# Kernel tuning notes

Hardware: AMD Instinct MI355X
Metric: run time of the kernel (lower is better)

## Reference

```python
import jax, jax.numpy as jnp
import numpy as np

H, L, N = 128, 8192, 64


def setup_inputs() -> dict:
    key = jax.random.key(0)
    ks = jax.random.split(key, 8)
    u = jax.random.normal(ks[0], (H, L), jnp.float32)
    # lecun_normal-scaled params, per channel
    Ct_ri = jax.random.normal(ks[1], (H, N, 2), jnp.float32) / np.sqrt(N)
    B_raw = jax.random.normal(ks[2], (H, N, 1), jnp.float32) / np.sqrt(N)
    D = jax.random.uniform(ks[3], (H,), jnp.float32)
    lo, hi = np.log(0.001), np.log(0.1)
    log_step = jax.random.uniform(ks[4], (H,), jnp.float32) * (hi - lo) + lo
    n = np.arange(N, dtype=np.float32)
    Lambda_re = jnp.full((N,), -0.5, jnp.float32)
    Lambda_im = jnp.asarray(np.pi * n, jnp.float32)
    p_re = jnp.asarray(np.sqrt(n + 0.5), jnp.float32)
    p_im = jnp.zeros((N,), jnp.float32)
    q_re = jnp.asarray(np.sqrt(n + 0.5), jnp.float32)
    q_im = jnp.zeros((N,), jnp.float32)
    Vc_re = jax.random.normal(ks[5], (N, N), jnp.float32) / np.sqrt(N)
    Vc_im = jax.random.normal(ks[6], (N, N), jnp.float32) / np.sqrt(N)
    return dict(u=u, Ct_ri=Ct_ri, B_raw=B_raw, D=D, log_step=log_step,
                Lambda_re=Lambda_re, Lambda_im=Lambda_im,
                p_re=p_re, p_im=p_im, q_re=q_re, q_im=q_im,
                Vc_re=Vc_re, Vc_im=Vc_im)


def _s4_forward(u, Ct_ri, B_raw, D, log_step,
                Lambda_re, Lambda_im, p_re, p_im, q_re, q_im, Vc_re, Vc_im):
    h, l = u.shape
    Lambda = (Lambda_re + 1j * Lambda_im).astype(jnp.complex64)   # (N,)
    p = (p_re + 1j * p_im).astype(jnp.complex64)                  # (N,)
    q = (q_re + 1j * q_im).astype(jnp.complex64)                  # (N,)
    Vc = (Vc_re + 1j * Vc_im).astype(jnp.complex64)               # (N,N)
    Ct = (Ct_ri[..., 0] + 1j * Ct_ri[..., 1]).astype(jnp.complex64)  # (H,N)
    # B = Vc @ B_raw  per channel -> (H,N)
    B = jnp.einsum('nm,hm->hn', Vc, B_raw[..., 0].astype(jnp.complex64))
    step = jnp.exp(log_step)                                      # (H,)

    # K_gen_DPLR evaluated at the L roots of unity (conv_from_gen)
    omega = jnp.exp(-2j * jnp.pi * (jnp.arange(l) / l)).astype(jnp.complex64)  # (L,)
    g = (2.0 / step)[:, None] * ((1.0 - omega) / (1.0 + omega))[None, :]       # (H,L)
    c = 2.0 / (1.0 + omega)                                                    # (L,)

    # cauchy_dot: sum_n a_n / (g - Lambda_n); reuse one (H,L,N) reciprocal
    recip = 1.0 / (g[:, :, None] - Lambda[None, None, :])          # (H,L,N)
    Ctc = Ct.conj()
    k00 = jnp.einsum('hn,hln->hl', Ctc * B, recip)
    k01 = jnp.einsum('hn,hln->hl', Ctc * p[None, :], recip)
    k10 = jnp.einsum('hn,hln->hl', q.conj()[None, :] * B, recip)
    k11 = jnp.einsum('n,hln->hl', q.conj() * p, recip)
    at_roots = c[None, :] * (k00 - k01 * (1.0 / (1.0 + k11)) * k10)  # (H,L)

    K = jnp.fft.ifft(at_roots, n=l, axis=-1).real                 # (H,L)

    # non_circular_convolution via zero-padded rfft
    ud = jnp.fft.rfft(jnp.pad(u, ((0, 0), (0, l))), axis=-1)
    Kd = jnp.fft.rfft(jnp.pad(K, ((0, 0), (0, l))), axis=-1)
    y = jnp.fft.irfft(ud * Kd, axis=-1)[:, :l]                    # (H,L)
    return y + D[:, None] * u


def reference(u, Ct_ri, B_raw, D, log_step,
              Lambda_re, Lambda_im, p_re, p_im, q_re, q_im, Vc_re, Vc_im):
    return _s4_forward(u, Ct_ri, B_raw, D, log_step,
                       Lambda_re, Lambda_im, p_re, p_im, q_re, q_im,
                       Vc_re, Vc_im)
```

## Files before the change

### kernel.cpp

```cpp
#include <hip/hip_runtime.h>
#include <math.h>

#define H 128
#define L 8192
#define NSTATE 64
#define NTH 1024
#define PI_D 3.14159265358979323846
#define RT2 0.70710678118654752440f

#define W16K_RE 0.99999992646571789f
#define W16K_IM (-3.8349518757139556e-4f)
#define W32K_RE 0.99999998161642898f
#define W32K_IM (-1.9174759731070332e-4f)

typedef float v2f __attribute__((ext_vector_type(2)));

__device__ __forceinline__ v2f pkfma(v2f a, v2f b, v2f c) {
    return __builtin_elementwise_fma(a, b, c);
}
__device__ __forceinline__ v2f pkfma(float a, v2f b, v2f c) {
    v2f av = a; return __builtin_elementwise_fma(av, b, c);
}

__device__ __forceinline__ int SWZ(int e) { return e ^ ((e >> 3) & 7); }
__device__ __forceinline__ int TSW(int j) { return j ^ ((j >> 4) & 15) ^ ((j >> 8) & 15); }
__device__ __forceinline__ int brev13(int x) { return (int)(__brev((unsigned)x) >> 19); }

__device__ __forceinline__ float2 cmul(float2 a, float2 b) {
    return make_float2(a.x * b.x - a.y * b.y, a.x * b.y + a.y * b.x);
}
__device__ __forceinline__ float2 cmulc(float2 w, float2 x) {
    return make_float2(w.x * x.x + w.y * x.y, w.x * x.y - w.y * x.x);
}
__device__ __forceinline__ float2 cadd(float2 a, float2 b) { return make_float2(a.x + b.x, a.y + b.y); }
__device__ __forceinline__ float2 csub(float2 a, float2 b) { return make_float2(a.x - b.x, a.y - b.y); }
__device__ __forceinline__ float2 mnegi(float2 a) { return make_float2(a.y, -a.x); }
__device__ __forceinline__ float2 mposi(float2 a) { return make_float2(-a.y, a.x); }

template<bool INV>
__device__ __forceinline__ float2 twget(const float2* __restrict__ tw, int idx) {
    float2 w;
    if (idx < 2048) w = tw[TSW(idx)];
    else { float2 t = tw[TSW(idx - 2048)]; w = make_float2(t.y, -t.x); }
    if (INV) w.y = -w.y;
    return w;
}

template<int SIGMA>
__device__ __forceinline__ void dif_pass1(float2* __restrict__ A,
                                          const float2* __restrict__ tw, int tid) {
    const int m1 = 2048 / SIGMA;
    #pragma unroll
    for (int rep = 0; rep < 2; ++rep) {
        int q = tid + rep * NTH;
        int r = q & (SIGMA - 1);
        int b = ((q & ~(SIGMA - 1)) << 2) | r;
        float2 w1 = tw[TSW(r * m1)];
        float2 w2 = cmul(w1, w1);
        float2 w1b = mnegi(w1);
        int i0 = SWZ(b), i1 = SWZ(b + SIGMA), i2 = SWZ(b + 2 * SIGMA), i3 = SWZ(b + 3 * SIGMA);
        float2 x0 = A[i0], x1 = A[i1], x2 = A[i2], x3 = A[i3];
        float2 y0 = cadd(x0, x2), y2 = cmul(csub(x0, x2), w1);
        float2 y1 = cadd(x1, x3), y3 = cmul(csub(x1, x3), w1b);
        A[i0] = cadd(y0, y1); A[i1] = cmul(csub(y0, y1), w2);
        A[i2] = cadd(y2, y3); A[i3] = cmul(csub(y2, y3), w2);
    }
}

template<int SIGMA>
__device__ __forceinline__ void dit_pass1(float2* __restrict__ A,
                                          const float2* __restrict__ tw, int tid) {
    const int m1 = 2048 / SIGMA;
    #pragma unroll
    for (int rep = 0; rep < 2; ++rep) {
        int q = tid + rep * NTH;
        int r = q & (SIGMA - 1);
        int b = ((q & ~(SIGMA - 1)) << 2) | r;
        float2 v1 = tw[TSW(r * m1)];
        float2 v2 = cmul(v1, v1);
        int i0 = SWZ(b), i1 = SWZ(b + SIGMA), i2 = SWZ(b + 2 * SIGMA), i3 = SWZ(b + 3 * SIGMA);
        float2 x0 = A[i0], x1 = A[i1], x2 = A[i2], x3 = A[i3];
        float2 t1 = cmulc(v2, x1);
        float2 y0 = cadd(x0, t1), y1 = csub(x0, t1);
        float2 t3 = cmulc(v2, x3);
        float2 y2 = cadd(x2, t3), y3 = csub(x2, t3);
        float2 u2 = cmulc(v1, y2);
        A[i0] = cadd(y0, u2); A[i2] = csub(y0, u2);
        float2 u3 = mposi(cmulc(v1, y3));
        A[i1] = cadd(y1, u3); A[i3] = csub(y1, u3);
    }
}

__global__ __launch_bounds__(NSTATE)
void s4_prep(const float* __restrict__ Ct_ri, const float* __restrict__ B_raw,
             const float* __restrict__ Lre_g, const float* __restrict__ Lim_g,
             const float* __restrict__ p_re, const float* __restrict__ p_im,
             const float* __restrict__ q_re, const float* __restrict__ q_im,
             const float* __restrict__ Vc_re, const float* __restrict__ Vc_im,
             char* __restrict__ ws)
{
    const int h = blockIdx.x, n = threadIdx.x;
    float2 Bc = make_float2(0.f, 0.f);
    for (int m = 0; m < NSTATE; ++m) {
        float br = B_raw[h * NSTATE + m];
        Bc.x += Vc_re[n * NSTATE + m] * br;
        Bc.y += Vc_im[n * NSTATE + m] * br;
    }
    float2 Ctc = make_float2(Ct_ri[(h * NSTATE + n) * 2 + 0],
                             -Ct_ri[(h * NSTATE + n) * 2 + 1]);
    float2 pc = make_float2(p_re[n], p_im[n]);
    float2 qc = make_float2(q_re[n], -q_im[n]);
    float2 w00 = cmul(Ctc, Bc);
    float2 w01 = cmul(Ctc, pc);
    float2 w10 = cmul(qc, Bc);
    float2 w11 = cmul(qc, pc);
    float dre = -Lre_g[n];
    float4* wq = (float4*)ws;
    float2* wr = (float2*)(ws + (size_t)H * NSTATE * 16);
    float4* wp = (float4*)(ws + (size_t)H * NSTATE * 24);
    wq[h * NSTATE + n] = make_float4(w00.x, w00.y, w01.x, w01.y);
    wr[h * NSTATE + n] = make_float2(w10.x, w10.y);
    wp[h * NSTATE + n] = make_float4(dre, dre * dre, Lim_g[n], w11.x);
}

__global__ __launch_bounds__(256)
void s4_combine(float4* __restrict__ out, const float4* __restrict__ yneg) {
    int i = blockIdx.x * 256 + threadIdx.x;
    float4 a = out[i], b = yneg[i];
    out[i] = make_float4(a.x + b.x, a.y + b.y, a.z + b.z, a.w + b.w);
}

extern __shared__ char smem_raw[];

template<bool WG, bool SP>
__global__ __launch_bounds__(NTH)
void s4_split_kernel(const float* __restrict__ u,
                     const float* __restrict__ Ct_ri,
                     const float* __restrict__ B_raw,
                     const float* __restrict__ Dp,
                     const float* __restrict__ log_step,
                     const float* __restrict__ Lre_g,
                     const float* __restrict__ Lim_g,
                     const float* __restrict__ p_re,
                     const float* __restrict__ p_im,
                     const float* __restrict__ q_re,
                     const float* __restrict__ q_im,
                     const float* __restrict__ Vc_re,
                     const float* __restrict__ Vc_im,
                     const char* __restrict__ wsw,
                     float* __restrict__ yneg,
                     float* __restrict__ out)
{
    float2* bufA   = (float2*)smem_raw;
    float2* tw     = bufA + L;
    float*  specRe = (float*)(tw + 2048);
    float*  specIm = specRe + L;
    float4* wq4    = (float4*)(specIm + L);
    float2* wr2    = (float2*)(wq4 + NSTATE);
    float4* wp4    = (float4*)(wr2 + NSTATE);

    const int bid  = blockIdx.x;
    const int type = bid >> 7;
    const int h    = bid & (H - 1);
    const int tid  = threadIdx.x;

    for (int j = tid; j < 2048; j += NTH) {
        double a = -2.0 * PI_D * (double)j / (double)L;
        tw[TSW(j)] = make_float2((float)cos(a), (float)sin(a));
    }
    const float4* wqg = nullptr; const float2* wrg = nullptr; const float4* wpg = nullptr;
    if constexpr (WG) {
        wqg = (const float4*)wsw + (size_t)h * NSTATE;
        wrg = (const float2*)(wsw + (size_t)H * NSTATE * 16) + (size_t)h * NSTATE;
        wpg = (const float4*)(wsw + (size_t)H * NSTATE * 24) + (size_t)h * NSTATE;
    } else {
        if (tid < NSTATE) {
            int n = tid;
            float2 Bc = make_float2(0.f, 0.f);
            for (int m = 0; m < NSTATE; ++m) {
                float br = B_raw[h * NSTATE + m];
                Bc.x += Vc_re[n * NSTATE + m] * br;
                Bc.y += Vc_im[n * NSTATE + m] * br;
            }
            float2 Ctc = make_float2(Ct_ri[(h * NSTATE + n) * 2 + 0],
                                     -Ct_ri[(h * NSTATE + n) * 2 + 1]);
            float2 pc = make_float2(p_re[n], p_im[n]);
            float2 qc = make_float2(q_re[n], -q_im[n]);
            float2 w00 = cmul(Ctc, Bc);
            float2 w01 = cmul(Ctc, pc);
            float2 w10 = cmul(qc, Bc);
            float2 w11 = cmul(qc, pc);
            float dre = -Lre_g[n];
            wq4[n] = make_float4(w00.x, w00.y, w01.x, w01.y);
            wr2[n] = make_float2(w10.x, w10.y);
            wp4[n] = make_float4(dre, dre * dre, Lim_g[n], w11.x);
        }
    }
    __syncthreads();

    const float step = expf(log_step[h]);
    const float two_over_step = 2.0f / step;
    const float Dh = Dp[h];
    const float* ur = u + (size_t)h * L;
    const float2 W16K = make_float2(W16K_RE, W16K_IM);
    const float2 W32K = make_float2(W32K_RE, W32K_IM);

    for (int i = tid; i < L; i += NTH) {
        float uv = ur[i];
        if (type == 0) {
            bufA[SWZ(i)] = make_float2(uv, 0.f);
        } else {
            float2 w = twget<false>(tw, i >> 1);
            if (i & 1) w = cmul(w, W16K);
            bufA[SWZ(i)] = make_float2(uv * w.x, uv * w.y);
        }
    }
    __syncthreads();

    dif_pass1<2048>(bufA, tw, tid); __syncthreads();
    dif_pass1<512>(bufA, tw, tid);  __syncthreads();
    dif_pass1<128>(bufA, tw, tid);  __syncthreads();
    dif_pass1<32>(bufA, tw, tid);   __syncthreads();
    dif_pass1<8>(bufA, tw, tid);    __syncthreads();

    #pragma unroll
    for (int p = 0; p < 4; ++p) {
        float tk0, tk1;
        v2f gv;
        #pragma unroll
        for (int e = 0; e < 2; ++e) {
            int k = brev13(8 * tid + 2 * p + e);
            float2 w;
            if (e == 0) {
                w = tw[TSW(k >> 1)];
            } else {
                float2 t0 = tw[TSW((k >> 1) - 2048)];
                w = make_float2(t0.y, -t0.x);
            }
            if (k & 1) w = cmul(w, W16K);
            if (type)  w = cmul(w, W32K);
            float t = -w.y * __builtin_amdgcn_rcpf(w.x);
            t = fminf(fmaxf(t, -3.0e7f), 3.0e7f);
            if (e == 0) { tk0 = t; gv.x = two_over_step * t; }
            else        { tk1 = t; gv.y = two_over_step * t; }
        }
        v2f A00x = 0.f, A00y = 0.f, A01x = 0.f, A01y = 0.f;
        v2f A10x = 0.f, A10y = 0.f, A11x = 0.f, A11y = 0.f;
        #pragma unroll 2
        for (int n = 0; n < NSTATE; ++n) {
            float4 qv = WG ? wqg[n] : wq4[n];
            float2 rv = WG ? wrg[n] : wr2[n];
            float4 pv = WG ? wpg[n] : wp4[n];
            v2f dim = gv - pv.z;
            v2f dre2 = pv.y;
            v2f den = pkfma(dim, dim, dre2);
            v2f inv; inv.x = __builtin_amdgcn_rcpf(den.x);
                     inv.y = __builtin_amdgcn_rcpf(den.y);
            v2f rre = pv.x * inv;
            v2f rim = -(dim * inv);
            A00x = pkfma(qv.x, rre, pkfma(-qv.y, rim, A00x));
            A00y = pkfma(qv.x, rim, pkfma( qv.y, rre, A00y));
            A01x = pkfma(qv.z, rre, pkfma(-qv.w, rim, A01x));
            A01y = pkfma(qv.z, rim, pkfma( qv.w, rre, A01y));
            A10x = pkfma(rv.x, rre, pkfma(-rv.y, rim, A10x));
            A10y = pkfma(rv.x, rim, pkfma( rv.y, rre, A10y));
            A11x = pkfma(pv.w, rre, A11x);
            A11y = pkfma(pv.w, rim, A11y);
        }
        #pragma unroll
        for (int e = 0; e < 2; ++e) {
            float2 a00 = make_float2(e ? A00x.y : A00x.x, e ? A00y.y : A00y.x);
            float2 a01 = make_float2(e ? A01x.y : A01x.x, e ? A01y.y : A01y.x);
            float2 a10 = make_float2(e ? A10x.y : A10x.x, e ? A10y.y : A10y.x);
            float2 a11 = make_float2(e ? A11x.y : A11x.x, e ? A11y.y : A11y.x);
            float tt = e ? tk1 : tk0;
            float2 den1 = make_float2(1.0f + a11.x, a11.y);
            float invd = 1.0f / (den1.x * den1.x + den1.y * den1.y);
            float2 qn = cmul(a01, a10);
            float2 dv = make_float2((qn.x * den1.x + qn.y * den1.y) * invd,
                                    (qn.y * den1.x - qn.x * den1.y) * invd);
            float2 tmp = make_float2(a00.x - dv.x, a00.y - dv.y);
            float2 s = cmul(make_float2(1.0f, tt), tmp);
            int j = 2 * p + e;
            specRe[j * NTH + tid] = s.x;
            specIm[j * NTH + tid] = s.y;
        }
    }

    {
        const int base = tid * 8;
        float2 x0 = bufA[SWZ(base + 0)], x1 = bufA[SWZ(base + 1)];
        float2 x2 = bufA[SWZ(base + 2)], x3 = bufA[SWZ(base + 3)];
        float2 x4 = bufA[SWZ(base + 4)], x5 = bufA[SWZ(base + 5)];
        float2 x6 = bufA[SWZ(base + 6)], x7 = bufA[SWZ(base + 7)];
        float2 a0 = cadd(x0, x4), a1 = cadd(x1, x5), a2 = cadd(x2, x6), a3 = cadd(x3, x7);
        float2 s0 = csub(x0, x4), s1 = csub(x1, x5), s2 = csub(x2, x6), s3 = csub(x3, x7);
        float2 b0 = s0;
        float2 b1 = cmul(s1, make_float2(RT2, -RT2));
        float2 b2 = mnegi(s2);
        float2 b3 = cmul(s3, make_float2(-RT2, -RT2));
        float2 c0 = cadd(a0, a2), c2 = csub(a0, a2);
        float2 c1 = cadd(a1, a3), c3 = mnegi(csub(a1, a3));
        float2 d0 = cadd(b0, b2), d2 = csub(b0, b2);
        float2 d1 = cadd(b1, b3), d3 = mnegi(csub(b1, b3));
        float2 y0 = cadd(c0, c1), y1 = csub(c0, c1);
        float2 y2 = cadd(c2, c3), y3 = csub(c2, c3);
        float2 y4 = cadd(d0, d1), y5 = csub(d0, d1);
        float2 y6 = cadd(d2, d3), y7 = csub(d2, d3);
        y0 = cmul(y0, make_float2(specRe[0 * NTH + tid], specIm[0 * NTH + tid]));
        y1 = cmul(y1, make_float2(specRe[1 * NTH + tid], specIm[1 * NTH + tid]));
        y2 = cmul(y2, make_float2(specRe[2 * NTH + tid], specIm[2 * NTH + tid]));
        y3 = cmul(y3, make_float2(specRe[3 * NTH + tid], specIm[3 * NTH + tid]));
        y4 = cmul(y4, make_float2(specRe[4 * NTH + tid], specIm[4 * NTH + tid]));
        y5 = cmul(y5, make_float2(specRe[5 * NTH + tid], specIm[5 * NTH + tid]));
        y6 = cmul(y6, make_float2(specRe[6 * NTH + tid], specIm[6 * NTH + tid]));
        y7 = cmul(y7, make_float2(specRe[7 * NTH + tid], specIm[7 * NTH + tid]));
        float2 e0 = cadd(y0, y1), e1 = csub(y0, y1), e2 = cadd(y2, y3), e3 = csub(y2, y3);
        float2 e4 = cadd(y4, y5), e5 = csub(y4, y5), e6 = cadd(y6, y7), e7 = csub(y6, y7);
        float2 f0 = cadd(e0, e2), f2 = csub(e0, e2);
        float2 ti = mposi(e3); float2 f1 = cadd(e1, ti), f3 = csub(e1, ti);
        float2 f4 = cadd(e4, e6), f6 = csub(e4, e6);
        float2 tj = mposi(e7); float2 f5 = cadd(e5, tj), f7 = csub(e5, tj);
        float2 g4 = f4;
        float2 g5 = cmul(make_float2(RT2, RT2), f5);
        float2 g6 = mposi(f6);
        float2 g7 = cmul(make_float2(-RT2, RT2), f7);
        bufA[SWZ(base + 0)] = cadd(f0, g4); bufA[SWZ(base + 4)] = csub(f0, g4);
        bufA[SWZ(base + 1)] = cadd(f1, g5); bufA[SWZ(base + 5)] = csub(f1, g5);
        bufA[SWZ(base + 2)] = cadd(f2, g6); bufA[SWZ(base + 6)] = csub(f2, g6);
        bufA[SWZ(base + 3)] = cadd(f3, g7); bufA[SWZ(base + 7)] = csub(f3, g7);
    }
    __syncthreads();

    dit_pass1<8>(bufA, tw, tid);    __syncthreads();
    dit_pass1<32>(bufA, tw, tid);   __syncthreads();
    dit_pass1<128>(bufA, tw, tid);  __syncthreads();
    dit_pass1<512>(bufA, tw, tid);  __syncthreads();
    dit_pass1<2048>(bufA, tw, tid); __syncthreads();

    const float sc = 0.5f / (float)L;
    float* orow = out + (size_t)h * L;
    float* yrow = SP ? (yneg + (size_t)h * L) : nullptr;
    for (int t = tid; t < L; t += NTH) {
        float2 z = bufA[SWZ(t)];
        float val;
        if (type == 0) {
            val = z.x * sc + Dh * ur[t];
        } else {
            float2 w = twget<false>(tw, t >> 1);
            if (t & 1) w = cmul(w, W16K);
            val = (w.x * z.x + w.y * z.y) * sc;
        }
        if constexpr (SP) {
            if (type == 0) orow[t] = val; else yrow[t] = val;
        } else {
            atomicAdd(&orow[t], val);
        }
    }
}

extern "C" void kernel_launch(void* const* d_in, const int* in_sizes, int n_in,
                              void* d_out, int out_size, void* d_ws, size_t ws_size,
                              hipStream_t stream) {
    (void)in_sizes; (void)n_in; (void)out_size;
    const float* u        = (const float*)d_in[0];
    const float* Ct_ri    = (const float*)d_in[1];
    const float* B_raw    = (const float*)d_in[2];
    const float* Dp       = (const float*)d_in[3];
    const float* log_step = (const float*)d_in[4];
    const float* Lre      = (const float*)d_in[5];
    const float* Lim      = (const float*)d_in[6];
    const float* p_re     = (const float*)d_in[7];
    const float* p_im     = (const float*)d_in[8];
    const float* q_re     = (const float*)d_in[9];
    const float* q_im     = (const float*)d_in[10];
    const float* Vc_re    = (const float*)d_in[11];
    const float* Vc_im    = (const float*)d_in[12];
    float* out = (float*)d_out;

    const size_t needW = (size_t)H * NSTATE * (16 + 8 + 16);
    const size_t needY = needW + (size_t)H * L * sizeof(float);
    const bool wg = ws_size >= needW;
    const bool sp = ws_size >= needY;

    char*  wsw  = (char*)d_ws;
    float* yneg = (float*)((char*)d_ws + needW);

    const size_t smemW = (size_t)(L + 2048) * sizeof(float2)
                       + (size_t)2 * L * sizeof(float);
    const size_t smemL = smemW + NSTATE * (16 + 8 + 16);

    if (wg) {
        s4_prep<<<dim3(H), dim3(NSTATE), 0, stream>>>(
            Ct_ri, B_raw, Lre, Lim, p_re, p_im, q_re, q_im, Vc_re, Vc_im, wsw);
        if (sp) {
            hipFuncSetAttribute((const void*)s4_split_kernel<true, true>,
                                hipFuncAttributeMaxDynamicSharedMemorySize, (int)smemW);
            s4_split_kernel<true, true><<<dim3(2 * H), dim3(NTH), smemW, stream>>>(
                u, Ct_ri, B_raw, Dp, log_step, Lre, Lim,
                p_re, p_im, q_re, q_im, Vc_re, Vc_im, wsw, yneg, out);
            s4_combine<<<dim3((H * L) / (256 * 4)), dim3(256), 0, stream>>>(
                (float4*)out, (const float4*)yneg);
        } else {
            hipMemsetAsync(out, 0, (size_t)H * L * sizeof(float), stream);
            hipFuncSetAttribute((const void*)s4_split_kernel<true, false>,
                                hipFuncAttributeMaxDynamicSharedMemorySize, (int)smemW);
            s4_split_kernel<true, false><<<dim3(2 * H), dim3(NTH), smemW, stream>>>(
                u, Ct_ri, B_raw, Dp, log_step, Lre, Lim,
                p_re, p_im, q_re, q_im, Vc_re, Vc_im, wsw, nullptr, out);
        }
    } else {
        hipMemsetAsync(out, 0, (size_t)H * L * sizeof(float), stream);
        hipFuncSetAttribute((const void*)s4_split_kernel<false, false>,
                            hipFuncAttributeMaxDynamicSharedMemorySize, (int)smemL);
        s4_split_kernel<false, false><<<dim3(2 * H), dim3(NTH), smemL, stream>>>(
            u, Ct_ri, B_raw, Dp, log_step, Lre, Lim,
            p_re, p_im, q_re, q_im, Vc_re, Vc_im, nullptr, nullptr, out);
    }
}
```

Before: 80.97 us.

## Interleave Cauchy kernel chunks with FFT passes between barriers

Splits the four-chunk Cauchy evaluation loop into a templated helper. Each chunk now runs between successive FFT butterfly passes, inside the same barrier interval, instead of all four running after the FFT. This is meant to overlap the ALU-heavy Cauchy sums with the LDS-bound FFT passes, hiding barrier stalls and LDS latency. It also drops one __syncthreads when the weights come from global memory, at the cost of more register pressure and code size.

```diff
diff --git a/kernel.cpp b/kernel.cpp
--- a/kernel.cpp
+++ b/kernel.cpp
@@ -88,6 +88,78 @@
         A[i0] = cadd(y0, u2); A[i2] = csub(y0, u2);
         float2 u3 = mposi(cmulc(v1, y3));
         A[i1] = cadd(y1, u3); A[i3] = csub(y1, u3);
+    }
+}
+
+template<int P>
+__device__ __forceinline__ void cauchy_chunk(
+    const int type, const int tid, const float two_over_step,
+    const float2* __restrict__ tw,
+    const float4* __restrict__ wq, const float2* __restrict__ wr,
+    const float4* __restrict__ wp,
+    float* __restrict__ specRe, float* __restrict__ specIm)
+{
+    const float2 W16K = make_float2(W16K_RE, W16K_IM);
+    const float2 W32K = make_float2(W32K_RE, W32K_IM);
+    float tk0, tk1;
+    v2f gv;
+    #pragma unroll
+    for (int e = 0; e < 2; ++e) {
+        int k = brev13(8 * tid + 2 * P + e);
+        float2 w;
+        if (e == 0) {
+            w = tw[TSW(k >> 1)];
+        } else {
+            float2 t0 = tw[TSW((k >> 1) - 2048)];
+            w = make_float2(t0.y, -t0.x);
+        }
+        if (k & 1) w = cmul(w, W16K);
+        if (type)  w = cmul(w, W32K);
+        float t = -w.y * __builtin_amdgcn_rcpf(w.x);
+        t = fminf(fmaxf(t, -3.0e7f), 3.0e7f);
+        if (e == 0) { tk0 = t; gv.x = two_over_step * t; }
+        else        { tk1 = t; gv.y = two_over_step * t; }
+    }
+    v2f A00x = 0.f, A00y = 0.f, A01x = 0.f, A01y = 0.f;
+    v2f A10x = 0.f, A10y = 0.f, A11x = 0.f, A11y = 0.f;
+    #pragma unroll 2
+    for (int n = 0; n < NSTATE; ++n) {
+        float4 qv = wq[n];
+        float2 rv = wr[n];
+        float4 pv = wp[n];
+        v2f dim = gv - pv.z;
+        v2f dre2 = pv.y;
+        v2f den = pkfma(dim, dim, dre2);
+        v2f inv; inv.x = __builtin_amdgcn_rcpf(den.x);
+                 inv.y = __builtin_amdgcn_rcpf(den.y);
+        v2f rre = pv.x * inv;
+        v2f rim = -(dim * inv);
+        A00x = pkfma(qv.x, rre, pkfma(-qv.y, rim, A00x));
+        A00y = pkfma(qv.x, rim, pkfma( qv.y, rre, A00y));
+        A01x = pkfma(qv.z, rre, pkfma(-qv.w, rim, A01x));
+        A01y = pkfma(qv.z, rim, pkfma( qv.w, rre, A01y));
+        A10x = pkfma(rv.x, rre, pkfma(-rv.y, rim, A10x));
+        A10y = pkfma(rv.x, rim, pkfma( rv.y, rre, A10y));
+        A11x = pkfma(pv.w, rre, A11x);
+        A11y = pkfma(pv.w, rim, A11y);
+    }
+    #pragma unroll
+    for (int e = 0; e < 2; ++e) {
+        float2 a00 = make_float2(e ? A00x.y : A00x.x, e ? A00y.y : A00y.x);
+        float2 a01 = make_float2(e ? A01x.y : A01x.x, e ? A01y.y : A01y.x);
+        float2 a10 = make_float2(e ? A10x.y : A10x.x, e ? A10y.y : A10y.x);
+        float2 a11 = make_float2(e ? A11x.y : A11x.x, e ? A11y.y : A11y.x);
+        float tt = e ? tk1 : tk0;
+        float2 den1 = make_float2(1.0f + a11.x, a11.y);
+        float invd = 1.0f / (den1.x * den1.x + den1.y * den1.y);
+        float2 qn = cmul(a01, a10);
+        float2 dv = make_float2((qn.x * den1.x + qn.y * den1.y) * invd,
+                                (qn.y * den1.x - qn.x * den1.y) * invd);
+        float2 tmp = make_float2(a00.x - dv.x, a00.y - dv.y);
+        float2 s = cmul(make_float2(1.0f, tt), tmp);
+        int j = 2 * P + e;
+        specRe[j * NTH + tid] = s.x;
+        specIm[j * NTH + tid] = s.y;
     }
 }
 
@@ -168,11 +240,11 @@
         double a = -2.0 * PI_D * (double)j / (double)L;
         tw[TSW(j)] = make_float2((float)cos(a), (float)sin(a));
     }
-    const float4* wqg = nullptr; const float2* wrg = nullptr; const float4* wpg = nullptr;
+    const float4* wqp; const float2* wrp; const float4* wpp;
     if constexpr (WG) {
-        wqg = (const float4*)wsw + (size_t)h * NSTATE;
-        wrg = (const float2*)(wsw + (size_t)H * NSTATE * 16) + (size_t)h * NSTATE;
-        wpg = (const float4*)(wsw + (size_t)H * NSTATE * 24) + (size_t)h * NSTATE;
+        wqp = (const float4*)wsw + (size_t)h * NSTATE;
+        wrp = (const float2*)(wsw + (size_t)H * NSTATE * 16) + (size_t)h * NSTATE;
+        wpp = (const float4*)(wsw + (size_t)H * NSTATE * 24) + (size_t)h * NSTATE;
     } else {
         if (tid < NSTATE) {
             int n = tid;
@@ -195,15 +267,15 @@
             wr2[n] = make_float2(w10.x, w10.y);
             wp4[n] = make_float4(dre, dre * dre, Lim_g[n], w11.x);
         }
-    }
-    __syncthreads();
+        wqp = wq4; wrp = wr2; wpp = wp4;
+    }
+    if constexpr (!WG) __syncthreads();
 
     const float step = expf(log_step[h]);
     const float two_over_step = 2.0f / step;
     const float Dh = Dp[h];
     const float* ur = u + (size_t)h * L;
     const float2 W16K = make_float2(W16K_RE, W16K_IM);
-    const float2 W32K = make_float2(W32K_RE, W32K_IM);
 
     for (int i = tid; i < L; i += NTH) {
         float uv = ur[i];
@@ -215,77 +287,20 @@
             bufA[SWZ(i)] = make_float2(uv * w.x, uv * w.y);
         }
     }
+    cauchy_chunk<0>(type, tid, two_over_step, tw, wqp, wrp, wpp, specRe, specIm);
     __syncthreads();
 
-    dif_pass1<2048>(bufA, tw, tid); __syncthreads();
-    dif_pass1<512>(bufA, tw, tid);  __syncthreads();
-    dif_pass1<128>(bufA, tw, tid);  __syncthreads();
+    dif_pass1<2048>(bufA, tw, tid);
+    cauchy_chunk<1>(type, tid, two_over_step, tw, wqp, wrp, wpp, specRe, specIm);
+    __syncthreads();
+    dif_pass1<512>(bufA, tw, tid);
+    cauchy_chunk<2>(type, tid, two_over_step, tw, wqp, wrp, wpp, specRe, specIm);
+    __syncthreads();
+    dif_pass1<128>(bufA, tw, tid);
+    cauchy_chunk<3>(type, tid, two_over_step, tw, wqp, wrp, wpp, specRe, specIm);
+    __syncthreads();
     dif_pass1<32>(bufA, tw, tid);   __syncthreads();
     dif_pass1<8>(bufA, tw, tid);    __syncthreads();
-
-    #pragma unroll
-    for (int p = 0; p < 4; ++p) {
-        float tk0, tk1;
-        v2f gv;
-        #pragma unroll
-        for (int e = 0; e < 2; ++e) {
-            int k = brev13(8 * tid + 2 * p + e);
-            float2 w;
-            if (e == 0) {
-                w = tw[TSW(k >> 1)];
-            } else {
-                float2 t0 = tw[TSW((k >> 1) - 2048)];
-                w = make_float2(t0.y, -t0.x);
-            }
-            if (k & 1) w = cmul(w, W16K);
-            if (type)  w = cmul(w, W32K);
-            float t = -w.y * __builtin_amdgcn_rcpf(w.x);
-            t = fminf(fmaxf(t, -3.0e7f), 3.0e7f);
-            if (e == 0) { tk0 = t; gv.x = two_over_step * t; }
-            else        { tk1 = t; gv.y = two_over_step * t; }
-        }
-        v2f A00x = 0.f, A00y = 0.f, A01x = 0.f, A01y = 0.f;
-        v2f A10x = 0.f, A10y = 0.f, A11x = 0.f, A11y = 0.f;
-        #pragma unroll 2
-        for (int n = 0; n < NSTATE; ++n) {
-            float4 qv = WG ? wqg[n] : wq4[n];
-            float2 rv = WG ? wrg[n] : wr2[n];
-            float4 pv = WG ? wpg[n] : wp4[n];
-            v2f dim = gv - pv.z;
-            v2f dre2 = pv.y;
-            v2f den = pkfma(dim, dim, dre2);
-            v2f inv; inv.x = __builtin_amdgcn_rcpf(den.x);
-                     inv.y = __builtin_amdgcn_rcpf(den.y);
-            v2f rre = pv.x * inv;
-            v2f rim = -(dim * inv);
-            A00x = pkfma(qv.x, rre, pkfma(-qv.y, rim, A00x));
-            A00y = pkfma(qv.x, rim, pkfma( qv.y, rre, A00y));
-            A01x = pkfma(qv.z, rre, pkfma(-qv.w, rim, A01x));
-            A01y = pkfma(qv.z, rim, pkfma( qv.w, rre, A01y));
-            A10x = pkfma(rv.x, rre, pkfma(-rv.y, rim, A10x));
-            A10y = pkfma(rv.x, rim, pkfma( rv.y, rre, A10y));
-            A11x = pkfma(pv.w, rre, A11x);
-            A11y = pkfma(pv.w, rim, A11y);
-        }
-        #pragma unroll
-        for (int e = 0; e < 2; ++e) {
-            float2 a00 = make_float2(e ? A00x.y : A00x.x, e ? A00y.y : A00y.x);
-            float2 a01 = make_float2(e ? A01x.y : A01x.x, e ? A01y.y : A01y.x);
-            float2 a10 = make_float2(e ? A10x.y : A10x.x, e ? A10y.y : A10y.x);
-            float2 a11 = make_float2(e ? A11x.y : A11x.x, e ? A11y.y : A11y.x);
-            float tt = e ? tk1 : tk0;
-            float2 den1 = make_float2(1.0f + a11.x, a11.y);
-            float invd = 1.0f / (den1.x * den1.x + den1.y * den1.y);
-            float2 qn = cmul(a01, a10);
-            float2 dv = make_float2((qn.x * den1.x + qn.y * den1.y) * invd,
-                                    (qn.y * den1.x - qn.x * den1.y) * invd);
-            float2 tmp = make_float2(a00.x - dv.x, a00.y - dv.y);
-            float2 s = cmul(make_float2(1.0f, tt), tmp);
-            int j = 2 * p + e;
-            specRe[j * NTH + tid] = s.x;
-            specIm[j * NTH + tid] = s.y;
-        }
-    }
 
     {
         const int base = tid * 8;
```

Result: no change. 80.45 us (-0.6%).
